# Kernel optimization log

Hardware: AMD Instinct MI355X
Metric: run time of the kernel (lower is better)

Reference implementation:

```python
import jax, jax.numpy as jnp
import numpy as np

B, T, C = 4, 2048, 2048  # batch, n_target, n_context
KEY_SIZE = 1024
VALUE_SIZE = 1024
NUM_HEADS = 16
KEY_HIDDEN = 64
HEAD_SIZE = VALUE_SIZE // NUM_HEADS  # 64
NORMALISE = True


def setup_inputs() -> dict:
    key = jax.random.key(0)
    ks = jax.random.split(key, 7)
    s = 0.02
    return {
        "queries": jax.random.normal(ks[0], (B, T, KEY_SIZE), jnp.float32),
        "keys": jax.random.normal(ks[1], (B, C, KEY_SIZE), jnp.float32),
        "values": jax.random.normal(ks[2], (B, C, VALUE_SIZE), jnp.float32),
        "Wq": jax.random.normal(ks[3], (NUM_HEADS * KEY_HIDDEN, KEY_SIZE), jnp.float32) * s,
        "Wk": jax.random.normal(ks[4], (NUM_HEADS * KEY_HIDDEN, KEY_SIZE), jnp.float32) * s,
        "Wv": jax.random.normal(ks[5], (NUM_HEADS * HEAD_SIZE, VALUE_SIZE), jnp.float32) * s,
        "Wo": jax.random.normal(ks[6], (VALUE_SIZE, NUM_HEADS * HEAD_SIZE), jnp.float32) * s,
    }


def reference(queries, keys, values, Wq, Wk, Wv, Wo):
    # Linear projections (torch nn.Linear: x @ W.T), reshape to heads
    q = (queries @ Wq.T).reshape(B, T, NUM_HEADS, KEY_HIDDEN)   # [B,T,H,Dk]
    k = (keys @ Wk.T).reshape(B, C, NUM_HEADS, KEY_HIDDEN)      # [B,C,H,Dk]
    v = (values @ Wv.T).reshape(B, C, NUM_HEADS, HEAD_SIZE)     # [B,C,H,Dv]
    scale = np.sqrt(KEY_HIDDEN).astype(np.float32)
    # Scores [B,H,T,C]
    scores = jnp.einsum('bthd,bchd->bhtc', q, k) / scale
    if NORMALISE:
        attn = jax.nn.softmax(scores, axis=-1)
    else:
        attn = jax.nn.sigmoid(scores)
    out = jnp.einsum('bhtc,bchd->bthd', attn, v)                # [B,T,H,Dv]
    out = out.reshape(B, T, NUM_HEADS * HEAD_SIZE)
    return out @ Wo.T                                            # [B,T,VALUE_SIZE]
```

## Files before the change

kernel.cpp:

```cpp
#include <hip/hip_runtime.h>
#include <stdint.h>

#define BATCH 4
#define SEQ   2048
#define EMB   1024
#define NH    16
#define HD    64

typedef __attribute__((ext_vector_type(4))) float  floatx4;
typedef __attribute__((ext_vector_type(8))) short  shortx8;

__device__ __forceinline__ unsigned short f2bf(float f) {
  unsigned u = __builtin_bit_cast(unsigned, f);
  u += 0x7FFFu + ((u >> 16) & 1u);
  return (unsigned short)(u >> 16);
}

__device__ __forceinline__ unsigned pack2bf(float a, float b) {
  return (unsigned)f2bf(a) | ((unsigned)f2bf(b) << 16);
}

__device__ __forceinline__ unsigned packtrunc(float a, float b) {
#if __has_builtin(__builtin_amdgcn_perm)
  return __builtin_amdgcn_perm(__builtin_bit_cast(unsigned, b),
                               __builtin_bit_cast(unsigned, a), 0x07060302u);
#else
  return (__builtin_bit_cast(unsigned, a) >> 16) |
         (__builtin_bit_cast(unsigned, b) & 0xFFFF0000u);
#endif
}

__device__ __forceinline__ float fexp2(float x) {
#if __has_builtin(__builtin_amdgcn_exp2f)
  return __builtin_amdgcn_exp2f(x);
#else
  return exp2f(x);
#endif
}

__device__ __forceinline__ void gl_lds16(const void* g, void* l) {
  __builtin_amdgcn_global_load_lds((const __attribute__((address_space(1))) void*)g,
                                   (__attribute__((address_space(3))) void*)l,
                                   16, 0, 0);
}

__device__ __forceinline__ void cast_body(const float* __restrict__ in,
                                          unsigned short* __restrict__ out, int bb, int t) {
  size_t i = (size_t)bb * 256 + t;
  const float4* p = (const float4*)in + i * 2;
  float4 f0 = p[0], f1 = p[1];
  uint4 o;
  o.x = pack2bf(f0.x, f0.y);
  o.y = pack2bf(f0.z, f0.w);
  o.z = pack2bf(f1.x, f1.y);
  o.w = pack2bf(f1.z, f1.w);
  ((uint4*)out)[i] = o;
}

__global__ __launch_bounds__(256) void cast_bf16(const float* __restrict__ in,
                                                 unsigned short* __restrict__ out) {
  cast_body(in, out, blockIdx.x, threadIdx.x);
}

__global__ __launch_bounds__(256) void cast3(const float* __restrict__ q, const float* __restrict__ k,
                                             const float* __restrict__ v,
                                             unsigned short* __restrict__ oq, unsigned short* __restrict__ ok,
                                             unsigned short* __restrict__ ov) {
  const float* in = blockIdx.y == 0 ? q : (blockIdx.y == 1 ? k : v);
  unsigned short* out = blockIdx.y == 0 ? oq : (blockIdx.y == 1 ? ok : ov);
  cast_body(in, out, blockIdx.x, threadIdx.x);
}

__global__ __launch_bounds__(256) void cast_w4(const float* __restrict__ i0, const float* __restrict__ i1,
                                               const float* __restrict__ i2, const float* __restrict__ i3,
                                               unsigned short* __restrict__ o0, unsigned short* __restrict__ o1,
                                               unsigned short* __restrict__ o2, unsigned short* __restrict__ o3) {
  int bb = blockIdx.x;
  const float* in; unsigned short* out;
  if      (bb < 512)  { in = i0; out = o0; }
  else if (bb < 1024) { in = i1; out = o1; bb -= 512; }
  else if (bb < 1536) { in = i2; out = o2; bb -= 1024; }
  else                { in = i3; out = o3; bb -= 1536; }
  cast_body(in, out, bb, threadIdx.x);
}

template <bool CF32>
__device__ __forceinline__ void gemm_body(const unsigned short* __restrict__ A,
                                          const unsigned short* __restrict__ Bt,
                                          void* __restrict__ Cp, float cscale) {
  constexpr int N = EMB, K = EMB;
  constexpr int BM = 128, BN = 128, BK = 32;
  __shared__ unsigned short As[BM * BK];
  __shared__ unsigned short Bs[BN * BK];
  const int t = threadIdx.x, w = t >> 6, lane = t & 63;
  const int quad = lane >> 4, lrow = lane & 15;
  const int m0 = blockIdx.y * BM, n0 = blockIdx.x * BN;
  const int wm = (w >> 1) * 64, wn = (w & 1) * 64;
  floatx4 acc[4][4] = {};

  for (int k0 = 0; k0 < K; k0 += BK) {
#pragma unroll
    for (int i = 0; i < 2; i++) {
      int q = i * 256 + t;
      int r = q >> 2, ce = (q & 3) * 8;
      gl_lds16(A + (size_t)(m0 + r) * K + k0 + ce, (char*)As + (size_t)(i * 256 + w * 64) * 16);
      gl_lds16(Bt + (size_t)(n0 + r) * K + k0 + ce, (char*)Bs + (size_t)(i * 256 + w * 64) * 16);
    }
    __syncthreads();
    shortx8 a[4];
#pragma unroll
    for (int mi = 0; mi < 4; mi++)
      a[mi] = *(const shortx8*)(As + (wm + mi * 16 + lrow) * BK + quad * 8);
#pragma unroll
    for (int ni = 0; ni < 4; ni++) {
      shortx8 b = *(const shortx8*)(Bs + (wn + ni * 16 + lrow) * BK + quad * 8);
#pragma unroll
      for (int mi = 0; mi < 4; mi++)
        acc[mi][ni] = __builtin_amdgcn_mfma_f32_16x16x32_bf16(a[mi], b, acc[mi][ni], 0, 0, 0);
    }
    __syncthreads();
  }
#pragma unroll
  for (int mi = 0; mi < 4; mi++)
#pragma unroll
    for (int ni = 0; ni < 4; ni++)
#pragma unroll
      for (int r = 0; r < 4; r++) {
        int row = m0 + wm + mi * 16 + quad * 4 + r;
        int col = n0 + wn + ni * 16 + lrow;
        float v = acc[mi][ni][r] * cscale;
        if constexpr (CF32) ((float*)Cp)[(size_t)row * N + col] = v;
        else                ((unsigned short*)Cp)[(size_t)row * N + col] = f2bf(v);
      }
}

__global__ __launch_bounds__(256, 2) void gemm_qkv(
    const unsigned short* __restrict__ Xq, const unsigned short* __restrict__ Xk,
    const unsigned short* __restrict__ Xv,
    const unsigned short* __restrict__ Wq, const unsigned short* __restrict__ Wk,
    const unsigned short* __restrict__ Wv,
    unsigned short* __restrict__ Oq, unsigned short* __restrict__ Ok,
    unsigned short* __restrict__ Ov, float sq) {
  const unsigned short *A, *Bt; unsigned short* C; float sc;
  if (blockIdx.z == 0)      { A = Xq; Bt = Wq; C = Oq; sc = sq; }
  else if (blockIdx.z == 1) { A = Xk; Bt = Wk; C = Ok; sc = 1.0f; }
  else                      { A = Xv; Bt = Wv; C = Ov; sc = 1.0f; }
  gemm_body<false>(A, Bt, C, sc);
}

__global__ __launch_bounds__(256, 2) void gemm_o(const unsigned short* __restrict__ A,
                                                 const unsigned short* __restrict__ Bt,
                                                 float* __restrict__ C) {
  gemm_body<true>(A, Bt, C, 1.0f);
}

__global__ __launch_bounds__(256) void transpose_v(const unsigned short* __restrict__ vp,
                                                   unsigned short* __restrict__ vT) {
  __shared__ unsigned short tile[64][72];
  const int c0 = blockIdx.x * 64, h = blockIdx.y, b = blockIdx.z;
  const int t = threadIdx.x;
#pragma unroll
  for (int i = 0; i < 2; i++) {
    int q = t + 256 * i;
    int r = q >> 3, dc = (q & 7) * 8;
    uint4 v = *(const uint4*)(vp + ((size_t)(b * SEQ + c0 + r)) * EMB + h * HD + dc);
    *(uint4*)&tile[r][dc] = v;
  }
  __syncthreads();
#pragma unroll
  for (int i = 0; i < 2; i++) {
    int q = t + 256 * i;
    int d = q >> 3, a = q & 7;
    unsigned e[8];
#pragma unroll
    for (int u = 0; u < 8; u++) {
      int cp = 8 * a + u;
      int c = 32 * (cp >> 5) + 16 * (cp & 1) + ((cp & 31) >> 1);
      e[u] = tile[c][d];
    }
    uint4 o;
    o.x = e[0] | (e[1] << 16); o.y = e[2] | (e[3] << 16);
    o.z = e[4] | (e[5] << 16); o.w = e[6] | (e[7] << 16);
    *(uint4*)(vT + ((size_t)((b * NH + h) * HD + d)) * SEQ + c0 + 8 * a) = o;
  }
}

__global__ __launch_bounds__(256, 4) void flash_attn(const unsigned short* __restrict__ qp,
                                                     const unsigned short* __restrict__ kp,
                                                     const unsigned short* __restrict__ vT,
                                                     unsigned short* __restrict__ ao) {
  __shared__ unsigned short Qs[128 * 64];
  __shared__ unsigned short Ks[64 * 64];
  __shared__ unsigned short Vts[64 * 64];
  __shared__ unsigned short Ps[4][16 * 40];
  const int t0 = blockIdx.x * 128, h = blockIdx.y, b = blockIdx.z;
  const int t = threadIdx.x, w = t >> 6, lane = t & 63;
  const int quad = lane >> 4, lrow = lane & 15;

#pragma unroll
  for (int i = 0; i < 4; i++) {
    int p = i * 256 + t;
    int r = p >> 3, kc = (p & 7) ^ (r & 7);
    gl_lds16(qp + ((size_t)(b * SEQ + t0 + r)) * EMB + h * HD + kc * 8,
             (char*)Qs + (size_t)(i * 256 + w * 64) * 16);
  }

  const unsigned short* ksrc[2];
  const unsigned short* vsrc[2];
#pragma unroll
  for (int i = 0; i < 2; i++) {
    int p = i * 256 + t;
    int r = p >> 3, kc = (p & 7) ^ (r & 7);
    ksrc[i] = kp + ((size_t)(b * SEQ + r)) * EMB + h * HD + kc * 8;
    vsrc[i] = vT + ((size_t)((b * NH + h) * HD + r)) * SEQ + kc * 8;
  }

  float l_st[2][4] = {};
  floatx4 accO[2][4] = {};

  for (int c0 = 0; c0 < SEQ; c0 += 64) {
    __syncthreads();
#pragma unroll
    for (int i = 0; i < 2; i++) {
      gl_lds16(ksrc[i], (char*)Ks + (size_t)(i * 256 + w * 64) * 16);
      gl_lds16(vsrc[i], (char*)Vts + (size_t)(i * 256 + w * 64) * 16);
      ksrc[i] += 64 * EMB;
      vsrc[i] += 64;
    }
    __syncthreads();

    floatx4 accS[2][4] = {};
#pragma unroll
    for (int kk = 0; kk < 2; kk++) {
      int qk = quad + kk * 4;
      shortx8 afr[2];
#pragma unroll
      for (int mi = 0; mi < 2; mi++) {
        int row = w * 32 + mi * 16 + lrow;
        afr[mi] = *(const shortx8*)(Qs + row * 64 + ((qk ^ (row & 7)) * 8));
      }
#pragma unroll
      for (int ni = 0; ni < 4; ni++) {
        int rowb = ni * 16 + lrow;
        shortx8 bfr = *(const shortx8*)(Ks + rowb * 64 + ((qk ^ (rowb & 7)) * 8));
#pragma unroll
        for (int mi = 0; mi < 2; mi++)
          accS[mi][ni] = __builtin_amdgcn_mfma_f32_16x16x32_bf16(afr[mi], bfr, accS[mi][ni], 0, 0, 0);
      }
    }

#pragma unroll
    for (int hh = 0; hh < 2; hh++) {
      shortx8 pafr[2];
#pragma unroll
      for (int mi = 0; mi < 2; mi++) {
#pragma unroll
        for (int r = 0; r < 4; r++) {
          float p0 = fexp2(accS[mi][2 * hh][r]);
          float p1 = fexp2(accS[mi][2 * hh + 1][r]);
          l_st[mi][r] += p0 + p1;
          *(unsigned*)(&Ps[w][(quad * 4 + r) * 40 + lrow * 2]) = packtrunc(p0, p1);
        }
        pafr[mi] = *(const shortx8*)(&Ps[w][lrow * 40 + quad * 8]);
      }
#pragma unroll
      for (int nio = 0; nio < 4; nio++) {
        int d = nio * 16 + lrow;
        shortx8 bfr = *(const shortx8*)(Vts + d * 64 + ((((hh << 2) + quad) ^ (d & 7)) * 8));
#pragma unroll
        for (int mi = 0; mi < 2; mi++)
          accO[mi][nio] = __builtin_amdgcn_mfma_f32_16x16x32_bf16(pafr[mi], bfr, accO[mi][nio], 0, 0, 0);
      }
    }
  }

#pragma unroll
  for (int mi = 0; mi < 2; mi++)
#pragma unroll
    for (int r = 0; r < 4; r++) {
      float l = l_st[mi][r];
      l += __shfl_xor(l, 1);
      l += __shfl_xor(l, 2);
      l += __shfl_xor(l, 4);
      l += __shfl_xor(l, 8);
      float inv = 1.0f / l;
#pragma unroll
      for (int nio = 0; nio < 4; nio++) accO[mi][nio][r] *= inv;
    }
#pragma unroll
  for (int mi = 0; mi < 2; mi++)
#pragma unroll
    for (int nio = 0; nio < 4; nio++)
#pragma unroll
      for (int r = 0; r < 4; r++) {
        int row = t0 + w * 32 + mi * 16 + quad * 4 + r;
        int col = h * HD + nio * 16 + lrow;
        ao[((size_t)(b * SEQ + row)) * EMB + col] = f2bf(accO[mi][nio][r]);
      }
}

extern "C" void kernel_launch(void* const* d_in, const int* in_sizes, int n_in,
                              void* d_out, int out_size, void* d_ws, size_t ws_size,
                              hipStream_t stream) {
  const float* queries = (const float*)d_in[0];
  const float* keys    = (const float*)d_in[1];
  const float* values  = (const float*)d_in[2];
  const float* Wq      = (const float*)d_in[3];
  const float* Wk      = (const float*)d_in[4];
  const float* Wv      = (const float*)d_in[5];
  const float* Wo      = (const float*)d_in[6];

  char* ws = (char*)d_ws;
  const size_t MB = 1ull << 20;
  const float SC2 = 0.125f * 1.44269504088896341f;

  unsigned short* wq_b = (unsigned short*)(ws + 0 * MB);
  unsigned short* wk_b = (unsigned short*)(ws + 2 * MB);
  unsigned short* wv_b = (unsigned short*)(ws + 4 * MB);
  unsigned short* wo_b = (unsigned short*)(ws + 6 * MB);

  cast_w4<<<2048, 256, 0, stream>>>(Wq, Wk, Wv, Wo, wq_b, wk_b, wv_b, wo_b);

  dim3 gg(EMB / 128, (BATCH * SEQ) / 128);

  if (ws_size >= 104 * MB) {
    unsigned short* Xq = (unsigned short*)(ws + 8 * MB);
    unsigned short* Xk = (unsigned short*)(ws + 24 * MB);
    unsigned short* Xv = (unsigned short*)(ws + 40 * MB);
    unsigned short* qp = (unsigned short*)(ws + 56 * MB);
    unsigned short* kp = (unsigned short*)(ws + 72 * MB);
    unsigned short* vp = (unsigned short*)(ws + 88 * MB);
    unsigned short* vT = Xk;
    unsigned short* ao = Xq;

    cast3<<<dim3(4096, 3), 256, 0, stream>>>(queries, keys, values, Xq, Xk, Xv);
    gemm_qkv<<<dim3(gg.x, gg.y, 3), 256, 0, stream>>>(Xq, Xk, Xv, wq_b, wk_b, wv_b,
                                                      qp, kp, vp, SC2);
    transpose_v<<<dim3(SEQ / 64, NH, BATCH), 256, 0, stream>>>(vp, vT);
    flash_attn<<<dim3(SEQ / 128, NH, BATCH), 256, 0, stream>>>(qp, kp, vT, ao);
    gemm_o<<<gg, 256, 0, stream>>>(ao, wo_b, (float*)d_out);
  } else {
    unsigned short* X  = (unsigned short*)(ws + 8 * MB);
    unsigned short* qp = (unsigned short*)(ws + 24 * MB);
    unsigned short* kp = (unsigned short*)(ws + 40 * MB);
    unsigned short* vp = (unsigned short*)(ws + 56 * MB);
    unsigned short* vT = (unsigned short*)(ws + 72 * MB);
    unsigned short* ao = X;

    cast_bf16<<<4096, 256, 0, stream>>>(queries, X);
    gemm_qkv<<<dim3(gg.x, gg.y, 1), 256, 0, stream>>>(X, X, X, wq_b, wq_b, wq_b,
                                                      qp, qp, qp, SC2);
    cast_bf16<<<4096, 256, 0, stream>>>(keys, X);
    gemm_qkv<<<dim3(gg.x, gg.y, 1), 256, 0, stream>>>(X, X, X, wk_b, wk_b, wk_b,
                                                      kp, kp, kp, 1.0f);
    cast_bf16<<<4096, 256, 0, stream>>>(values, X);
    gemm_qkv<<<dim3(gg.x, gg.y, 1), 256, 0, stream>>>(X, X, X, wv_b, wv_b, wv_b,
                                                      vp, vp, vp, 1.0f);
    transpose_v<<<dim3(SEQ / 64, NH, BATCH), 256, 0, stream>>>(vp, vT);
    flash_attn<<<dim3(SEQ / 128, NH, BATCH), 256, 0, stream>>>(qp, kp, vT, ao);
    gemm_o<<<gg, 256, 0, stream>>>(ao, wo_b, (float*)d_out);
  }
}
```

Baseline: 344.6 us.

## Double-buffer flash attention K/V, widen GEMM BK with swizzle, fuse casts

```diff
diff --git a/kernel.cpp b/kernel.cpp
--- a/kernel.cpp
+++ b/kernel.cpp
@@ -62,13 +62,23 @@
   cast_body(in, out, blockIdx.x, threadIdx.x);
 }
 
-__global__ __launch_bounds__(256) void cast3(const float* __restrict__ q, const float* __restrict__ k,
-                                             const float* __restrict__ v,
-                                             unsigned short* __restrict__ oq, unsigned short* __restrict__ ok,
-                                             unsigned short* __restrict__ ov) {
-  const float* in = blockIdx.y == 0 ? q : (blockIdx.y == 1 ? k : v);
-  unsigned short* out = blockIdx.y == 0 ? oq : (blockIdx.y == 1 ? ok : ov);
-  cast_body(in, out, blockIdx.x, threadIdx.x);
+__global__ __launch_bounds__(256) void cast_all(
+    const float* __restrict__ q, const float* __restrict__ k, const float* __restrict__ v,
+    const float* __restrict__ w0, const float* __restrict__ w1,
+    const float* __restrict__ w2, const float* __restrict__ w3,
+    unsigned short* __restrict__ oq, unsigned short* __restrict__ ok, unsigned short* __restrict__ ov,
+    unsigned short* __restrict__ ow0, unsigned short* __restrict__ ow1,
+    unsigned short* __restrict__ ow2, unsigned short* __restrict__ ow3) {
+  int bb = blockIdx.x;
+  const float* in; unsigned short* out;
+  if      (bb < 4096)  { in = q;  out = oq; }
+  else if (bb < 8192)  { in = k;  out = ok;  bb -= 4096; }
+  else if (bb < 12288) { in = v;  out = ov;  bb -= 8192; }
+  else if (bb < 12800) { in = w0; out = ow0; bb -= 12288; }
+  else if (bb < 13312) { in = w1; out = ow1; bb -= 12800; }
+  else if (bb < 13824) { in = w2; out = ow2; bb -= 13312; }
+  else                 { in = w3; out = ow3; bb -= 13824; }
+  cast_body(in, out, bb, threadIdx.x);
 }
 
 __global__ __launch_bounds__(256) void cast_w4(const float* __restrict__ i0, const float* __restrict__ i1,
@@ -89,7 +99,7 @@
                                           const unsigned short* __restrict__ Bt,
                                           void* __restrict__ Cp, float cscale) {
   constexpr int N = EMB, K = EMB;
-  constexpr int BM = 128, BN = 128, BK = 32;
+  constexpr int BM = 128, BN = 128, BK = 64;
   __shared__ unsigned short As[BM * BK];
   __shared__ unsigned short Bs[BN * BK];
   const int t = threadIdx.x, w = t >> 6, lane = t & 63;
@@ -98,25 +108,40 @@
   const int wm = (w >> 1) * 64, wn = (w & 1) * 64;
   floatx4 acc[4][4] = {};
 
+  const unsigned short* asrc[4];
+  const unsigned short* bsrc[4];
+#pragma unroll
+  for (int i = 0; i < 4; i++) {
+    int q = i * 256 + t;
+    int r = q >> 3, kc = (q & 7) ^ (r & 7);
+    asrc[i] = A + (size_t)(m0 + r) * K + kc * 8;
+    bsrc[i] = Bt + (size_t)(n0 + r) * K + kc * 8;
+  }
+
   for (int k0 = 0; k0 < K; k0 += BK) {
 #pragma unroll
-    for (int i = 0; i < 2; i++) {
-      int q = i * 256 + t;
-      int r = q >> 2, ce = (q & 3) * 8;
-      gl_lds16(A + (size_t)(m0 + r) * K + k0 + ce, (char*)As + (size_t)(i * 256 + w * 64) * 16);
-      gl_lds16(Bt + (size_t)(n0 + r) * K + k0 + ce, (char*)Bs + (size_t)(i * 256 + w * 64) * 16);
+    for (int i = 0; i < 4; i++) {
+      gl_lds16(asrc[i], (char*)As + (size_t)(i * 256 + w * 64) * 16);
+      gl_lds16(bsrc[i], (char*)Bs + (size_t)(i * 256 + w * 64) * 16);
+      asrc[i] += BK; bsrc[i] += BK;
     }
     __syncthreads();
-    shortx8 a[4];
-#pragma unroll
-    for (int mi = 0; mi < 4; mi++)
-      a[mi] = *(const shortx8*)(As + (wm + mi * 16 + lrow) * BK + quad * 8);
-#pragma unroll
-    for (int ni = 0; ni < 4; ni++) {
-      shortx8 b = *(const shortx8*)(Bs + (wn + ni * 16 + lrow) * BK + quad * 8);
-#pragma unroll
-      for (int mi = 0; mi < 4; mi++)
-        acc[mi][ni] = __builtin_amdgcn_mfma_f32_16x16x32_bf16(a[mi], b, acc[mi][ni], 0, 0, 0);
+#pragma unroll
+    for (int ks = 0; ks < 2; ks++) {
+      shortx8 a[4];
+#pragma unroll
+      for (int mi = 0; mi < 4; mi++) {
+        int row = wm + mi * 16 + lrow;
+        a[mi] = *(const shortx8*)(As + row * 64 + (((ks * 4 + quad) ^ (row & 7)) * 8));
+      }
+#pragma unroll
+      for (int ni = 0; ni < 4; ni++) {
+        int rowb = wn + ni * 16 + lrow;
+        shortx8 b = *(const shortx8*)(Bs + rowb * 64 + (((ks * 4 + quad) ^ (rowb & 7)) * 8));
+#pragma unroll
+        for (int mi = 0; mi < 4; mi++)
+          acc[mi][ni] = __builtin_amdgcn_mfma_f32_16x16x32_bf16(a[mi], b, acc[mi][ni], 0, 0, 0);
+      }
     }
     __syncthreads();
   }
@@ -185,13 +210,13 @@
   }
 }
 
-__global__ __launch_bounds__(256, 4) void flash_attn(const unsigned short* __restrict__ qp,
+__global__ __launch_bounds__(256, 3) void flash_attn(const unsigned short* __restrict__ qp,
                                                      const unsigned short* __restrict__ kp,
                                                      const unsigned short* __restrict__ vT,
                                                      unsigned short* __restrict__ ao) {
   __shared__ unsigned short Qs[128 * 64];
-  __shared__ unsigned short Ks[64 * 64];
-  __shared__ unsigned short Vts[64 * 64];
+  __shared__ unsigned short Ks[2][64 * 64];
+  __shared__ unsigned short Vts[2][64 * 64];
   __shared__ unsigned short Ps[4][16 * 40];
   const int t0 = blockIdx.x * 128, h = blockIdx.y, b = blockIdx.z;
   const int t = threadIdx.x, w = t >> 6, lane = t & 63;
@@ -215,19 +240,31 @@
     vsrc[i] = vT + ((size_t)((b * NH + h) * HD + r)) * SEQ + kc * 8;
   }
 
+#pragma unroll
+  for (int i = 0; i < 2; i++) {
+    gl_lds16(ksrc[i], (char*)Ks[0] + (size_t)(i * 256 + w * 64) * 16);
+    gl_lds16(vsrc[i], (char*)Vts[0] + (size_t)(i * 256 + w * 64) * 16);
+    ksrc[i] += 64 * EMB;
+    vsrc[i] += 64;
+  }
+
   float l_st[2][4] = {};
   floatx4 accO[2][4] = {};
 
-  for (int c0 = 0; c0 < SEQ; c0 += 64) {
+  for (int it = 0; it < SEQ / 64; it++) {
+    const int cur = it & 1;
     __syncthreads();
-#pragma unroll
-    for (int i = 0; i < 2; i++) {
-      gl_lds16(ksrc[i], (char*)Ks + (size_t)(i * 256 + w * 64) * 16);
-      gl_lds16(vsrc[i], (char*)Vts + (size_t)(i * 256 + w * 64) * 16);
-      ksrc[i] += 64 * EMB;
-      vsrc[i] += 64;
-    }
-    __syncthreads();
+    if (it + 1 < SEQ / 64) {
+#pragma unroll
+      for (int i = 0; i < 2; i++) {
+        gl_lds16(ksrc[i], (char*)Ks[cur ^ 1] + (size_t)(i * 256 + w * 64) * 16);
+        gl_lds16(vsrc[i], (char*)Vts[cur ^ 1] + (size_t)(i * 256 + w * 64) * 16);
+        ksrc[i] += 64 * EMB;
+        vsrc[i] += 64;
+      }
+    }
+    const unsigned short* Kc = Ks[cur];
+    const unsigned short* Vc = Vts[cur];
 
     floatx4 accS[2][4] = {};
 #pragma unroll
@@ -242,7 +279,7 @@
 #pragma unroll
       for (int ni = 0; ni < 4; ni++) {
         int rowb = ni * 16 + lrow;
-        shortx8 bfr = *(const shortx8*)(Ks + rowb * 64 + ((qk ^ (rowb & 7)) * 8));
+        shortx8 bfr = *(const shortx8*)(Kc + rowb * 64 + ((qk ^ (rowb & 7)) * 8));
 #pragma unroll
         for (int mi = 0; mi < 2; mi++)
           accS[mi][ni] = __builtin_amdgcn_mfma_f32_16x16x32_bf16(afr[mi], bfr, accS[mi][ni], 0, 0, 0);
@@ -266,7 +303,7 @@
 #pragma unroll
       for (int nio = 0; nio < 4; nio++) {
         int d = nio * 16 + lrow;
-        shortx8 bfr = *(const shortx8*)(Vts + d * 64 + ((((hh << 2) + quad) ^ (d & 7)) * 8));
+        shortx8 bfr = *(const shortx8*)(Vc + d * 64 + ((((hh << 2) + quad) ^ (d & 7)) * 8));
 #pragma unroll
         for (int mi = 0; mi < 2; mi++)
           accO[mi][nio] = __builtin_amdgcn_mfma_f32_16x16x32_bf16(pafr[mi], bfr, accO[mi][nio], 0, 0, 0);
@@ -319,8 +356,6 @@
   unsigned short* wv_b = (unsigned short*)(ws + 4 * MB);
   unsigned short* wo_b = (unsigned short*)(ws + 6 * MB);
 
-  cast_w4<<<2048, 256, 0, stream>>>(Wq, Wk, Wv, Wo, wq_b, wk_b, wv_b, wo_b);
-
   dim3 gg(EMB / 128, (BATCH * SEQ) / 128);
 
   if (ws_size >= 104 * MB) {
@@ -333,7 +368,8 @@
     unsigned short* vT = Xk;
     unsigned short* ao = Xq;
 
-    cast3<<<dim3(4096, 3), 256, 0, stream>>>(queries, keys, values, Xq, Xk, Xv);
+    cast_all<<<14336, 256, 0, stream>>>(queries, keys, values, Wq, Wk, Wv, Wo,
+                                        Xq, Xk, Xv, wq_b, wk_b, wv_b, wo_b);
     gemm_qkv<<<dim3(gg.x, gg.y, 3), 256, 0, stream>>>(Xq, Xk, Xv, wq_b, wk_b, wv_b,
                                                       qp, kp, vp, SC2);
     transpose_v<<<dim3(SEQ / 64, NH, BATCH), 256, 0, stream>>>(vp, vT);
@@ -347,6 +383,7 @@
     unsigned short* vT = (unsigned short*)(ws + 72 * MB);
     unsigned short* ao = X;
 
+    cast_w4<<<2048, 256, 0, stream>>>(Wq, Wk, Wv, Wo, wq_b, wk_b, wv_b, wo_b);
     cast_bf16<<<4096, 256, 0, stream>>>(queries, X);
     gemm_qkv<<<dim3(gg.x, gg.y, 1), 256, 0, stream>>>(X, X, X, wq_b, wq_b, wq_b,
                                                       qp, qp, qp, SC2);
```

New measurement: 349.7 us. Within noise of the previous version (+1.5%).
